# Performance work log

Measured on AMD Instinct MI355X. Metric: run time of the kernel, lower is better.

The kernel has to match this reference:

```python
import jax, jax.numpy as jnp
import numpy as np

ALPHA = 0.1  # config['alpha']


def setup_inputs() -> dict:
    key = jax.random.key(0)
    k1, k2, k3, k4, k5 = jax.random.split(key, 5)
    n_bs, bit, n_cls, class_bit, n_train = 128, 48, 100, 16, 10000
    u = jax.random.normal(k1, (n_bs, bit), dtype=jnp.float32)
    # multi-hot labels (float, as in torch: y.float())
    y = jax.random.bernoulli(k2, 0.1, (n_bs, n_cls)).astype(jnp.float32)
    ind = jnp.arange(n_bs, dtype=jnp.int64)  # distinct in-range row indices
    # buffers mid-training: U holds previous class-wise codes, Y previous labels
    U = jax.random.normal(k3, (n_train, n_cls, class_bit), dtype=jnp.float32) * 0.1
    Y = jax.random.bernoulli(k4, 0.1, (n_train, n_cls)).astype(jnp.float32)
    # xavier_uniform-like init for w_D [n_class, bit, class_bit]
    limit = np.sqrt(6.0 / (bit + class_bit)).astype(np.float32)
    w_D = jax.random.uniform(k5, (n_cls, bit, class_bit), dtype=jnp.float32,
                             minval=-limit, maxval=limit)
    return {"u": u, "y": y, "ind": ind, "U": U, "Y": Y, "w_D": w_D}


def reference(u, y, ind, U, Y, w_D):
    # update label buffer: self.Y[ind, :] = y
    Y = Y.at[ind].set(y)
    # u_ = matmul(u, w_D).permute(1,0,2): [n_bs, n_cls, class_bit]
    u_ = jnp.einsum('bk,ckd->bcd', u, w_D)
    # update code buffer with detached u_ (torch: self.U[ind] = u_.data)
    U = U.at[ind].set(jax.lax.stop_gradient(u_))
    # pairwise similarity s: [n_bs, n_train, n_cls]
    s = y[:, None, :] * Y[None, :, :]
    # inner_product: sum over class_bit -> [n_bs, n_train, n_cls]
    ip = jnp.einsum('tcd,bcd->btc', U, u_)
    # stable log(1 + exp(ip)) - s*ip, exactly as the torch expression
    likelihood = (jnp.log1p(jnp.exp(-jnp.abs(ip))) + jnp.maximum(ip, 0.0)
                  - s * ip).mean()
    quantization = ALPHA * jnp.mean((u_ - jnp.sign(u_)) ** 2)
    return likelihood + quantization
```

## Files before the change

kernel.cpp:

```cpp
#include <hip/hip_runtime.h>
#include <math.h>

#define CB 16
#define ALPHA 0.1f
#define LOG2E 1.4426950408889634f
#define LN2F  0.6931471805599453f

typedef __bf16 bf16x8 __attribute__((ext_vector_type(8)));
typedef float  f32x16 __attribute__((ext_vector_type(16)));

__device__ inline float block_reduce_256(float v, float* red) {
    #pragma unroll
    for (int off = 32; off > 0; off >>= 1) v += __shfl_down(v, off, 64);
    int lane = threadIdx.x & 63;
    int wid  = threadIdx.x >> 6;
    if (lane == 0) red[wid] = v;
    __syncthreads();
    float s = 0.f;
    if (threadIdx.x == 0) {
        int nw = blockDim.x >> 6;
        for (int w = 0; w < nw; ++w) s += red[w];
    }
    return s;
}

__global__ __launch_bounds__(256) void prep_kernel(
        const float* __restrict__ u, const float* __restrict__ y,
        const float* __restrict__ w_D,
        float* __restrict__ u_f32, __bf16* __restrict__ u_bf,
        float* __restrict__ quant_partials,
        float* __restrict__ vvec, float* __restrict__ wvec,
        int n_bs, int bit, int n_cls, int nub) {
    __shared__ float red[4];
    __shared__ float yus[4][64];
    __shared__ float sus[4][64];
    if ((int)blockIdx.x < nub) {
        int idx = blockIdx.x * 256 + threadIdx.x;
        int total = n_bs * n_cls * CB;
        float q = 0.f;
        if (idx < total) {
            int d = idx & (CB - 1);
            int c = (idx / CB) % n_cls;
            int b = idx / (CB * n_cls);
            const float* __restrict__ ur = u + (size_t)b * bit;
            const float* __restrict__ w  = w_D + (size_t)c * bit * CB + d;
            float s = 0.f;
            for (int k = 0; k < bit; ++k) s = fmaf(ur[k], w[k * CB], s);
            u_f32[idx] = s;
            u_bf[((size_t)c * n_bs + b) * CB + d] = (__bf16)(s * LOG2E);
            float sgn = (s > 0.f) ? 1.f : ((s < 0.f) ? -1.f : 0.f);
            float dd = s - sgn;
            q = dd * dd;
        }
        float bs = block_reduce_256(q, red);
        if (threadIdx.x == 0) quant_partials[blockIdx.x] = bs;
    } else {
        const int c  = blockIdx.x - nub;
        const int kk = threadIdx.x & 63;
        const int sl = threadIdx.x >> 6;
        float yv = 0.f, sv = 0.f;
        if (kk < bit) {
            const int bpp = n_bs >> 2;
            for (int b = sl * bpp; b < (sl + 1) * bpp; ++b) {
                float uv = u[(size_t)b * bit + kk];
                sv += uv;
                yv = fmaf(y[(size_t)b * n_cls + c], uv, yv);
            }
        }
        yus[sl][kk] = yv; sus[sl][kk] = sv;
        __syncthreads();
        if (sl == 0 && kk < bit) {
            yus[0][kk] = yus[0][kk] + yus[1][kk] + yus[2][kk] + yus[3][kk];
            sus[0][kk] = sus[0][kk] + sus[1][kk] + sus[2][kk] + sus[3][kk];
        }
        __syncthreads();
        if (threadIdx.x < CB) {
            const int d = threadIdx.x;
            const float* __restrict__ wdc = w_D + (size_t)c * bit * CB + d;
            float v = 0.f, w = 0.f;
            for (int k = 0; k < bit; ++k) {
                float wv = wdc[k * CB];
                v = fmaf(yus[0][k], wv, v);
                w = fmaf(sus[0][k], wv, w);
            }
            vvec[(size_t)c * CB + d] = v;
            wvec[(size_t)c * CB + d] = w;
        }
    }
}

__global__ __launch_bounds__(256, 4) void loss_main_mfma(
        const float* __restrict__ y, const float* __restrict__ U,
        const float* __restrict__ Yb, const float* __restrict__ u_f32,
        const __bf16* __restrict__ u_bf,
        const float* __restrict__ vvec, const float* __restrict__ wvec,
        const int* __restrict__ ind, float* __restrict__ partials,
        int n_bs, int n_cls, int n_train) {
    __shared__ float red[4];
    __shared__ int pflag[32];
    const int tid  = threadIdx.x;
    const int lane = tid & 63;
    const int wid  = tid >> 6;
    const int c    = blockIdx.x * 4 + wid;
    const int t0   = blockIdx.y * 32;
    const int r    = lane & 31;
    const int h    = lane >> 5;
    const int row  = t0 + r;

    if (tid < 32) pflag[tid] = -1;

    const int rc = (row < n_train) ? row : (n_train - 1);
    const float* __restrict__ ar = U + ((size_t)rc * n_cls + c) * CB + h * 8;
    float4 a0 = *(const float4*)(ar);
    float4 a1 = *(const float4*)(ar + 4);
    float Yv = Yb[(size_t)rc * n_cls + c];

    __syncthreads();
    if (tid < n_bs) {
        unsigned rl = (unsigned)(ind[tid] - t0);
        if (rl < 32u) pflag[rl] = tid;
    }
    __syncthreads();

    const int pf = pflag[r];
    if (pf >= 0) {
        const float* __restrict__ src =
            u_f32 + ((size_t)pf * n_cls + c) * CB + h * 8;
        a0 = *(const float4*)(src);
        a1 = *(const float4*)(src + 4);
        Yv = y[(size_t)pf * n_cls + c];
    }
    if (row >= n_train) {
        a0 = make_float4(0.f, 0.f, 0.f, 0.f); a1 = a0; Yv = 0.f;
    }

    const float* __restrict__ vp = vvec + (size_t)c * CB + h * 8;
    const float* __restrict__ wp = wvec + (size_t)c * CB + h * 8;
    float sv = a0.x*vp[0] + a0.y*vp[1] + a0.z*vp[2] + a0.w*vp[3]
             + a1.x*vp[4] + a1.y*vp[5] + a1.z*vp[6] + a1.w*vp[7];
    float sw = a0.x*wp[0] + a0.y*wp[1] + a0.z*wp[2] + a0.w*wp[3]
             + a1.x*wp[4] + a1.y*wp[5] + a1.z*wp[6] + a1.w*wp[7];
    const float sideS = Yv * sv;
    const float sideW = sw;

    bf16x8 A;
    A[0] = (__bf16)a0.x; A[1] = (__bf16)a0.y;
    A[2] = (__bf16)a0.z; A[3] = (__bf16)a0.w;
    A[4] = (__bf16)a1.x; A[5] = (__bf16)a1.y;
    A[6] = (__bf16)a1.z; A[7] = (__bf16)a1.w;

    const __bf16* __restrict__ ub = u_bf + (size_t)c * n_bs * CB;
    bf16x8 B[4];
    #pragma unroll
    for (int bt = 0; bt < 4; ++bt)
        B[bt] = *(const bf16x8*)(ub + (size_t)(bt * 32 + r) * CB + h * 8);

    float accA = 0.f;
    float pp   = 1.f;
    f32x16 zc = {};
    #pragma unroll
    for (int bt = 0; bt < 4; ++bt) {
        f32x16 D = __builtin_amdgcn_mfma_f32_32x32x16_bf16(A, B[bt], zc, 0, 0, 0);
        float a[16];
        #pragma unroll
        for (int j = 0; j < 16; ++j) {
            float ipa = fabsf(D[j]);
            a[j] = 1.0f + __builtin_amdgcn_exp2f(-ipa);
            accA += ipa;
        }
        #pragma unroll
        for (int s = 1; s < 16; s <<= 1)
            #pragma unroll
            for (int j = 0; j < 16; j += 2 * s) a[j] *= a[j + s];
        pp *= a[0];
    }
    float accL = __builtin_amdgcn_logf(pp);

    float contrib = LN2F * accL + (0.5f * LN2F) * accA + 0.5f * sideW - sideS;

    #pragma unroll
    for (int off = 32; off > 0; off >>= 1)
        contrib += __shfl_down(contrib, off, 64);
    if (lane == 0) red[wid] = contrib;
    __syncthreads();
    if (tid == 0) {
        int bid = blockIdx.y * gridDim.x + blockIdx.x;
        partials[bid] = red[0] + red[1] + red[2] + red[3];
    }
}

__global__ __launch_bounds__(256) void finalize_kernel(
        const float* __restrict__ partials, int nblk,
        const float* __restrict__ quant_partials, int n_quant,
        float* __restrict__ out, double pad_corr,
        double like_scale, double quant_scale) {
    double s = 0.0, q = 0.0;
    for (int i = threadIdx.x; i < nblk; i += 256) s += (double)partials[i];
    for (int i = threadIdx.x; i < n_quant; i += 256) q += (double)quant_partials[i];
    #pragma unroll
    for (int off = 32; off > 0; off >>= 1) {
        s += __shfl_down(s, off, 64);
        q += __shfl_down(q, off, 64);
    }
    __shared__ double dred[4][2];
    int lane = threadIdx.x & 63, wid = threadIdx.x >> 6;
    if (lane == 0) { dred[wid][0] = s; dred[wid][1] = q; }
    __syncthreads();
    if (threadIdx.x == 0) {
        double S = dred[0][0] + dred[1][0] + dred[2][0] + dred[3][0];
        double Q = dred[0][1] + dred[1][1] + dred[2][1] + dred[3][1];
        out[0] = (float)((S - pad_corr) * like_scale + Q * quant_scale);
    }
}

extern "C" void kernel_launch(void* const* d_in, const int* in_sizes, int n_in,
                              void* d_out, int out_size, void* d_ws, size_t ws_size,
                              hipStream_t stream) {
    const float* u   = (const float*)d_in[0];
    const float* y   = (const float*)d_in[1];
    const int*   ind = (const int*)d_in[2];
    const float* U   = (const float*)d_in[3];
    const float* Yb  = (const float*)d_in[4];
    const float* w_D = (const float*)d_in[5];

    const int n_bs    = in_sizes[2];
    const int bit     = in_sizes[0] / n_bs;
    const int n_cls   = in_sizes[1] / n_bs;
    const int n_train = in_sizes[4] / n_cls;

    const int totalU = n_bs * n_cls * CB;
    const int nub    = (totalU + 255) / 256;
    const int ntile  = (n_train + 31) / 32;
    const int gx     = (n_cls + 3) / 4;
    const int nblk   = ntile * gx;

    char* ws = (char*)d_ws;
    size_t off = 0;
    float* u_f32 = (float*)(ws + off);          off += (size_t)totalU * 4;
    __bf16* u_bf = (__bf16*)(ws + off);         off += (size_t)totalU * 2;
    off = (off + 15) & ~(size_t)15;
    float* vvec = (float*)(ws + off);           off += (size_t)n_cls * CB * 4;
    float* wvec = (float*)(ws + off);           off += (size_t)n_cls * CB * 4;
    float* quant_partials = (float*)(ws + off); off += (size_t)nub * 4;
    off = (off + 15) & ~(size_t)15;
    float* partials = (float*)(ws + off);       off += (size_t)nblk * 4;

    prep_kernel<<<nub + n_cls, 256, 0, stream>>>(
        u, y, w_D, u_f32, u_bf, quant_partials, vvec, wvec,
        n_bs, bit, n_cls, nub);

    loss_main_mfma<<<dim3(gx, ntile), 256, 0, stream>>>(
        y, U, Yb, u_f32, u_bf, vvec, wvec, ind, partials,
        n_bs, n_cls, n_train);

    const double ln2 = 0.6931471805599453;
    const double n_pad = (double)((long long)(ntile * 32 - n_train) *
                                  (long long)n_bs * (long long)n_cls);
    const double pad_corr    = ln2 * n_pad;
    const double like_scale  = 1.0 / ((double)n_bs * n_train * n_cls);
    const double quant_scale = (double)ALPHA / (double)totalU;

    finalize_kernel<<<1, 256, 0, stream>>>(partials, nblk, quant_partials, nub,
                                           (float*)d_out, pad_corr,
                                           like_scale, quant_scale);
}
```

Measured before the change: 51.21 us.

## Process four train tiles per block with register prefetch of next tile

Each block now loops over four 32-row train tiles instead of one. It loads the B fragments and the v/w vectors once per block and prefetches the next tile's U rows and labels into registers while the current tile runs its MFMAs and transcendentals. This amortizes per-block setup (index scan, B loads, syncs) and overlaps global loads with compute. The cost is four times fewer blocks (around 2500 instead of about 7800), which may reduce latency hiding from occupancy, and extra register pressure.

```diff
diff --git a/kernel.cpp b/kernel.cpp
--- a/kernel.cpp
+++ b/kernel.cpp
@@ -5,6 +5,7 @@
 #define ALPHA 0.1f
 #define LOG2E 1.4426950408889634f
 #define LN2F  0.6931471805599453f
+#define NT 4
 
 typedef __bf16 bf16x8 __attribute__((ext_vector_type(8)));
 typedef float  f32x16 __attribute__((ext_vector_type(16)));
@@ -97,86 +98,111 @@
         const int* __restrict__ ind, float* __restrict__ partials,
         int n_bs, int n_cls, int n_train) {
     __shared__ float red[4];
-    __shared__ int pflag[32];
+    __shared__ int pflag[NT * 32];
     const int tid  = threadIdx.x;
     const int lane = tid & 63;
     const int wid  = tid >> 6;
     const int c    = blockIdx.x * 4 + wid;
-    const int t0   = blockIdx.y * 32;
+    const int bt0  = blockIdx.y * (NT * 32);
     const int r    = lane & 31;
     const int h    = lane >> 5;
-    const int row  = t0 + r;
-
-    if (tid < 32) pflag[tid] = -1;
-
-    const int rc = (row < n_train) ? row : (n_train - 1);
-    const float* __restrict__ ar = U + ((size_t)rc * n_cls + c) * CB + h * 8;
-    float4 a0 = *(const float4*)(ar);
-    float4 a1 = *(const float4*)(ar + 4);
-    float Yv = Yb[(size_t)rc * n_cls + c];
-
+
+    for (int i = tid; i < NT * 32; i += 256) pflag[i] = -1;
     __syncthreads();
     if (tid < n_bs) {
-        unsigned rl = (unsigned)(ind[tid] - t0);
-        if (rl < 32u) pflag[rl] = tid;
-    }
-    __syncthreads();
-
-    const int pf = pflag[r];
-    if (pf >= 0) {
-        const float* __restrict__ src =
-            u_f32 + ((size_t)pf * n_cls + c) * CB + h * 8;
-        a0 = *(const float4*)(src);
-        a1 = *(const float4*)(src + 4);
-        Yv = y[(size_t)pf * n_cls + c];
-    }
-    if (row >= n_train) {
-        a0 = make_float4(0.f, 0.f, 0.f, 0.f); a1 = a0; Yv = 0.f;
-    }
+        unsigned rl = (unsigned)(ind[tid] - bt0);
+        if (rl < (unsigned)(NT * 32)) pflag[rl] = tid;
+    }
+
+    const __bf16* __restrict__ ub = u_bf + (size_t)c * n_bs * CB;
+    bf16x8 B[4];
+    #pragma unroll
+    for (int bt = 0; bt < 4; ++bt)
+        B[bt] = *(const bf16x8*)(ub + (size_t)(bt * 32 + r) * CB + h * 8);
 
     const float* __restrict__ vp = vvec + (size_t)c * CB + h * 8;
     const float* __restrict__ wp = wvec + (size_t)c * CB + h * 8;
-    float sv = a0.x*vp[0] + a0.y*vp[1] + a0.z*vp[2] + a0.w*vp[3]
-             + a1.x*vp[4] + a1.y*vp[5] + a1.z*vp[6] + a1.w*vp[7];
-    float sw = a0.x*wp[0] + a0.y*wp[1] + a0.z*wp[2] + a0.w*wp[3]
-             + a1.x*wp[4] + a1.y*wp[5] + a1.z*wp[6] + a1.w*wp[7];
-    const float sideS = Yv * sv;
-    const float sideW = sw;
-
-    bf16x8 A;
-    A[0] = (__bf16)a0.x; A[1] = (__bf16)a0.y;
-    A[2] = (__bf16)a0.z; A[3] = (__bf16)a0.w;
-    A[4] = (__bf16)a1.x; A[5] = (__bf16)a1.y;
-    A[6] = (__bf16)a1.z; A[7] = (__bf16)a1.w;
-
-    const __bf16* __restrict__ ub = u_bf + (size_t)c * n_bs * CB;
-    bf16x8 B[4];
-    #pragma unroll
-    for (int bt = 0; bt < 4; ++bt)
-        B[bt] = *(const bf16x8*)(ub + (size_t)(bt * 32 + r) * CB + h * 8);
+    float4 vp0 = *(const float4*)(vp);
+    float4 vp1 = *(const float4*)(vp + 4);
+    float4 wp0 = *(const float4*)(wp);
+    float4 wp1 = *(const float4*)(wp + 4);
+
+    __syncthreads();
+
+    int rowp = bt0 + r;
+    int rcp  = (rowp < n_train) ? rowp : (n_train - 1);
+    const float* __restrict__ arp = U + ((size_t)rcp * n_cls + c) * CB + h * 8;
+    float4 a0c = *(const float4*)(arp);
+    float4 a1c = *(const float4*)(arp + 4);
+    float  Yvc = Yb[(size_t)rcp * n_cls + c];
 
     float accA = 0.f;
-    float pp   = 1.f;
+    float accL = 0.f;
+    float linC = 0.f;
     f32x16 zc = {};
-    #pragma unroll
-    for (int bt = 0; bt < 4; ++bt) {
-        f32x16 D = __builtin_amdgcn_mfma_f32_32x32x16_bf16(A, B[bt], zc, 0, 0, 0);
-        float a[16];
+
+    #pragma unroll
+    for (int it = 0; it < NT; ++it) {
+        float4 a0n, a1n; float Yvn = 0.f;
+        if (it + 1 < NT) {
+            int rown = bt0 + (it + 1) * 32 + r;
+            int rcn  = (rown < n_train) ? rown : (n_train - 1);
+            const float* __restrict__ arn =
+                U + ((size_t)rcn * n_cls + c) * CB + h * 8;
+            a0n = *(const float4*)(arn);
+            a1n = *(const float4*)(arn + 4);
+            Yvn = Yb[(size_t)rcn * n_cls + c];
+        }
+
+        const int pf = pflag[it * 32 + r];
+        if (pf >= 0) {
+            const float* __restrict__ src =
+                u_f32 + ((size_t)pf * n_cls + c) * CB + h * 8;
+            a0c = *(const float4*)(src);
+            a1c = *(const float4*)(src + 4);
+            Yvc = y[(size_t)pf * n_cls + c];
+        }
+        const int rowc = bt0 + it * 32 + r;
+        if (rowc >= n_train) {
+            a0c = make_float4(0.f, 0.f, 0.f, 0.f); a1c = a0c; Yvc = 0.f;
+        }
+
+        float sv = a0c.x*vp0.x + a0c.y*vp0.y + a0c.z*vp0.z + a0c.w*vp0.w
+                 + a1c.x*vp1.x + a1c.y*vp1.y + a1c.z*vp1.z + a1c.w*vp1.w;
+        float sw = a0c.x*wp0.x + a0c.y*wp0.y + a0c.z*wp0.z + a0c.w*wp0.w
+                 + a1c.x*wp1.x + a1c.y*wp1.y + a1c.z*wp1.z + a1c.w*wp1.w;
+        linC += 0.5f * sw - Yvc * sv;
+
+        bf16x8 A;
+        A[0] = (__bf16)a0c.x; A[1] = (__bf16)a0c.y;
+        A[2] = (__bf16)a0c.z; A[3] = (__bf16)a0c.w;
+        A[4] = (__bf16)a1c.x; A[5] = (__bf16)a1c.y;
+        A[6] = (__bf16)a1c.z; A[7] = (__bf16)a1c.w;
+
+        float pp = 1.f;
         #pragma unroll
-        for (int j = 0; j < 16; ++j) {
-            float ipa = fabsf(D[j]);
-            a[j] = 1.0f + __builtin_amdgcn_exp2f(-ipa);
-            accA += ipa;
-        }
-        #pragma unroll
-        for (int s = 1; s < 16; s <<= 1)
+        for (int bt = 0; bt < 4; ++bt) {
+            f32x16 D = __builtin_amdgcn_mfma_f32_32x32x16_bf16(A, B[bt], zc,
+                                                               0, 0, 0);
+            float a[16];
             #pragma unroll
-            for (int j = 0; j < 16; j += 2 * s) a[j] *= a[j + s];
-        pp *= a[0];
-    }
-    float accL = __builtin_amdgcn_logf(pp);
-
-    float contrib = LN2F * accL + (0.5f * LN2F) * accA + 0.5f * sideW - sideS;
+            for (int j = 0; j < 16; ++j) {
+                float ipa = fabsf(D[j]);
+                a[j] = 1.0f + __builtin_amdgcn_exp2f(-ipa);
+                accA += ipa;
+            }
+            #pragma unroll
+            for (int s = 1; s < 16; s <<= 1)
+                #pragma unroll
+                for (int j = 0; j < 16; j += 2 * s) a[j] *= a[j + s];
+            pp *= a[0];
+        }
+        accL += __builtin_amdgcn_logf(pp);
+
+        a0c = a0n; a1c = a1n; Yvc = Yvn;
+    }
+
+    float contrib = LN2F * accL + (0.5f * LN2F) * accA + linC;
 
     #pragma unroll
     for (int off = 32; off > 0; off >>= 1)
@@ -231,8 +257,9 @@
     const int totalU = n_bs * n_cls * CB;
     const int nub    = (totalU + 255) / 256;
     const int ntile  = (n_train + 31) / 32;
+    const int gy     = (ntile + NT - 1) / NT;
     const int gx     = (n_cls + 3) / 4;
-    const int nblk   = ntile * gx;
+    const int nblk   = gy * gx;
 
     char* ws = (char*)d_ws;
     size_t off = 0;
@@ -249,12 +276,12 @@
         u, y, w_D, u_f32, u_bf, quant_partials, vvec, wvec,
         n_bs, bit, n_cls, nub);
 
-    loss_main_mfma<<<dim3(gx, ntile), 256, 0, stream>>>(
+    loss_main_mfma<<<dim3(gx, gy), 256, 0, stream>>>(
         y, U, Yb, u_f32, u_bf, vvec, wvec, ind, partials,
         n_bs, n_cls, n_train);
 
     const double ln2 = 0.6931471805599453;
-    const double n_pad = (double)((long long)(ntile * 32 - n_train) *
+    const double n_pad = (double)((long long)(gy * NT * 32 - n_train) *
                                   (long long)n_bs * (long long)n_cls);
     const double pad_corr    = ln2 * n_pad;
     const double like_scale  = 1.0 / ((double)n_bs * n_train * n_cls);
```

New measurement: 201.3 us. +293.0%, slower.

## Make loss blocks persistent over multiple train tiles with per-wave partials

Applied to the files above, without the earlier changes.

Each block now loops over up to eight strided 32-row train tiles instead of handling one tile, so the grid shrinks from 313 to 40 rows of blocks. The B operand, the v/w vectors and the ind-to-row flag table are loaded once per block and reused across tiles. The final cross-wave LDS reduction and barrier are removed; each wave writes its own partial and the finalize kernel sums four times as many entries. Fewer blocks (25x40 = 1000) means less launch and setup overhead. The cost is less parallelism and a serial dependency chain per block, with no unrolling of the tile loop.

```diff
diff --git a/kernel.cpp b/kernel.cpp
--- a/kernel.cpp
+++ b/kernel.cpp
@@ -5,6 +5,7 @@
 #define ALPHA 0.1f
 #define LOG2E 1.4426950408889634f
 #define LN2F  0.6931471805599453f
+#define MAXW 8
 
 typedef __bf16 bf16x8 __attribute__((ext_vector_type(8)));
 typedef float  f32x16 __attribute__((ext_vector_type(16)));
@@ -95,97 +96,104 @@
         const __bf16* __restrict__ u_bf,
         const float* __restrict__ vvec, const float* __restrict__ wvec,
         const int* __restrict__ ind, float* __restrict__ partials,
-        int n_bs, int n_cls, int n_train) {
-    __shared__ float red[4];
-    __shared__ int pflag[32];
+        int n_bs, int n_cls, int n_train, int ntile, int GY) {
+    __shared__ int pflag[MAXW * 32];
     const int tid  = threadIdx.x;
     const int lane = tid & 63;
     const int wid  = tid >> 6;
     const int c    = blockIdx.x * 4 + wid;
-    const int t0   = blockIdx.y * 32;
+    const int by   = blockIdx.y;
     const int r    = lane & 31;
     const int h    = lane >> 5;
-    const int row  = t0 + r;
-
-    if (tid < 32) pflag[tid] = -1;
-
-    const int rc = (row < n_train) ? row : (n_train - 1);
-    const float* __restrict__ ar = U + ((size_t)rc * n_cls + c) * CB + h * 8;
-    float4 a0 = *(const float4*)(ar);
-    float4 a1 = *(const float4*)(ar + 4);
-    float Yv = Yb[(size_t)rc * n_cls + c];
-
+    const int nw   = (ntile - by + GY - 1) / GY;
+
+    for (int i = tid; i < MAXW * 32; i += 256) pflag[i] = -1;
     __syncthreads();
     if (tid < n_bs) {
-        unsigned rl = (unsigned)(ind[tid] - t0);
-        if (rl < 32u) pflag[rl] = tid;
-    }
-    __syncthreads();
-
-    const int pf = pflag[r];
-    if (pf >= 0) {
-        const float* __restrict__ src =
-            u_f32 + ((size_t)pf * n_cls + c) * CB + h * 8;
-        a0 = *(const float4*)(src);
-        a1 = *(const float4*)(src + 4);
-        Yv = y[(size_t)pf * n_cls + c];
-    }
-    if (row >= n_train) {
-        a0 = make_float4(0.f, 0.f, 0.f, 0.f); a1 = a0; Yv = 0.f;
-    }
-
+        int t = ind[tid];
+        for (int w = 0; w < nw; ++w) {
+            unsigned rl = (unsigned)(t - (by + w * GY) * 32);
+            if (rl < 32u) pflag[w * 32 + rl] = tid;
+        }
+    }
+    __syncthreads();
+
+    const __bf16* __restrict__ ub = u_bf + (size_t)c * n_bs * CB;
+    bf16x8 B[4];
+    #pragma unroll
+    for (int bt = 0; bt < 4; ++bt)
+        B[bt] = *(const bf16x8*)(ub + (size_t)(bt * 32 + r) * CB + h * 8);
     const float* __restrict__ vp = vvec + (size_t)c * CB + h * 8;
     const float* __restrict__ wp = wvec + (size_t)c * CB + h * 8;
-    float sv = a0.x*vp[0] + a0.y*vp[1] + a0.z*vp[2] + a0.w*vp[3]
-             + a1.x*vp[4] + a1.y*vp[5] + a1.z*vp[6] + a1.w*vp[7];
-    float sw = a0.x*wp[0] + a0.y*wp[1] + a0.z*wp[2] + a0.w*wp[3]
-             + a1.x*wp[4] + a1.y*wp[5] + a1.z*wp[6] + a1.w*wp[7];
-    const float sideS = Yv * sv;
-    const float sideW = sw;
-
-    bf16x8 A;
-    A[0] = (__bf16)a0.x; A[1] = (__bf16)a0.y;
-    A[2] = (__bf16)a0.z; A[3] = (__bf16)a0.w;
-    A[4] = (__bf16)a1.x; A[5] = (__bf16)a1.y;
-    A[6] = (__bf16)a1.z; A[7] = (__bf16)a1.w;
-
-    const __bf16* __restrict__ ub = u_bf + (size_t)c * n_bs * CB;
-    bf16x8 B[4];
-    #pragma unroll
-    for (int bt = 0; bt < 4; ++bt)
-        B[bt] = *(const bf16x8*)(ub + (size_t)(bt * 32 + r) * CB + h * 8);
-
-    float accA = 0.f;
-    float pp   = 1.f;
+    float4 vp0 = *(const float4*)(vp);
+    float4 vp1 = *(const float4*)(vp + 4);
+    float4 wp0 = *(const float4*)(wp);
+    float4 wp1 = *(const float4*)(wp + 4);
+
+    float acc = 0.f;
     f32x16 zc = {};
-    #pragma unroll
-    for (int bt = 0; bt < 4; ++bt) {
-        f32x16 D = __builtin_amdgcn_mfma_f32_32x32x16_bf16(A, B[bt], zc, 0, 0, 0);
-        float a[16];
+    #pragma unroll 1
+    for (int w = 0; w < nw; ++w) {
+        const int t0  = (by + w * GY) * 32;
+        const int row = t0 + r;
+        const int rc  = (row < n_train) ? row : (n_train - 1);
+        const float* __restrict__ ar = U + ((size_t)rc * n_cls + c) * CB + h * 8;
+        float4 a0 = *(const float4*)(ar);
+        float4 a1 = *(const float4*)(ar + 4);
+        float Yv = Yb[(size_t)rc * n_cls + c];
+
+        const int pf = pflag[w * 32 + r];
+        if (pf >= 0) {
+            const float* __restrict__ src =
+                u_f32 + ((size_t)pf * n_cls + c) * CB + h * 8;
+            a0 = *(const float4*)(src);
+            a1 = *(const float4*)(src + 4);
+            Yv = y[(size_t)pf * n_cls + c];
+        }
+        if (row >= n_train) {
+            a0 = make_float4(0.f, 0.f, 0.f, 0.f); a1 = a0; Yv = 0.f;
+        }
+
+        float sv = a0.x*vp0.x + a0.y*vp0.y + a0.z*vp0.z + a0.w*vp0.w
+                 + a1.x*vp1.x + a1.y*vp1.y + a1.z*vp1.z + a1.w*vp1.w;
+        float sw = a0.x*wp0.x + a0.y*wp0.y + a0.z*wp0.z + a0.w*wp0.w
+                 + a1.x*wp1.x + a1.y*wp1.y + a1.z*wp1.z + a1.w*wp1.w;
+
+        bf16x8 A;
+        A[0] = (__bf16)a0.x; A[1] = (__bf16)a0.y;
+        A[2] = (__bf16)a0.z; A[3] = (__bf16)a0.w;
+        A[4] = (__bf16)a1.x; A[5] = (__bf16)a1.y;
+        A[6] = (__bf16)a1.z; A[7] = (__bf16)a1.w;
+
+        float accA = 0.f;
+        float pp   = 1.f;
         #pragma unroll
-        for (int j = 0; j < 16; ++j) {
-            float ipa = fabsf(D[j]);
-            a[j] = 1.0f + __builtin_amdgcn_exp2f(-ipa);
-            accA += ipa;
-        }
-        #pragma unroll
-        for (int s = 1; s < 16; s <<= 1)
+        for (int bt = 0; bt < 4; ++bt) {
+            f32x16 D = __builtin_amdgcn_mfma_f32_32x32x16_bf16(A, B[bt], zc,
+                                                               0, 0, 0);
+            float a[16];
             #pragma unroll
-            for (int j = 0; j < 16; j += 2 * s) a[j] *= a[j + s];
-        pp *= a[0];
-    }
-    float accL = __builtin_amdgcn_logf(pp);
-
-    float contrib = LN2F * accL + (0.5f * LN2F) * accA + 0.5f * sideW - sideS;
+            for (int j = 0; j < 16; ++j) {
+                float ipa = fabsf(D[j]);
+                a[j] = 1.0f + __builtin_amdgcn_exp2f(-ipa);
+                accA += ipa;
+            }
+            #pragma unroll
+            for (int s = 1; s < 16; s <<= 1)
+                #pragma unroll
+                for (int j = 0; j < 16; j += 2 * s) a[j] *= a[j + s];
+            pp *= a[0];
+        }
+        float accL = __builtin_amdgcn_logf(pp);
+        acc += LN2F * accL + (0.5f * LN2F) * accA + 0.5f * sw - Yv * sv;
+    }
 
     #pragma unroll
     for (int off = 32; off > 0; off >>= 1)
-        contrib += __shfl_down(contrib, off, 64);
-    if (lane == 0) red[wid] = contrib;
-    __syncthreads();
-    if (tid == 0) {
-        int bid = blockIdx.y * gridDim.x + blockIdx.x;
-        partials[bid] = red[0] + red[1] + red[2] + red[3];
+        acc += __shfl_down(acc, off, 64);
+    if (lane == 0) {
+        int bid = by * gridDim.x + blockIdx.x;
+        partials[bid * 4 + wid] = acc;
     }
 }
 
@@ -231,8 +239,10 @@
     const int totalU = n_bs * n_cls * CB;
     const int nub    = (totalU + 255) / 256;
     const int ntile  = (n_train + 31) / 32;
+    const int GY     = (ntile + MAXW - 1) / MAXW;
     const int gx     = (n_cls + 3) / 4;
-    const int nblk   = ntile * gx;
+    const int nblk   = GY * gx;
+    const int npart  = nblk * 4;
 
     char* ws = (char*)d_ws;
     size_t off = 0;
@@ -243,15 +253,15 @@
     float* wvec = (float*)(ws + off);           off += (size_t)n_cls * CB * 4;
     float* quant_partials = (float*)(ws + off); off += (size_t)nub * 4;
     off = (off + 15) & ~(size_t)15;
-    float* partials = (float*)(ws + off);       off += (size_t)nblk * 4;
+    float* partials = (float*)(ws + off);       off += (size_t)npart * 4;
 
     prep_kernel<<<nub + n_cls, 256, 0, stream>>>(
         u, y, w_D, u_f32, u_bf, quant_partials, vvec, wvec,
         n_bs, bit, n_cls, nub);
 
-    loss_main_mfma<<<dim3(gx, ntile), 256, 0, stream>>>(
+    loss_main_mfma<<<dim3(gx, GY), 256, 0, stream>>>(
         y, U, Yb, u_f32, u_bf, vvec, wvec, ind, partials,
-        n_bs, n_cls, n_train);
+        n_bs, n_cls, n_train, ntile, GY);
 
     const double ln2 = 0.6931471805599453;
     const double n_pad = (double)((long long)(ntile * 32 - n_train) *
@@ -260,7 +270,7 @@
     const double like_scale  = 1.0 / ((double)n_bs * n_train * n_cls);
     const double quant_scale = (double)ALPHA / (double)totalU;
 
-    finalize_kernel<<<1, 256, 0, stream>>>(partials, nblk, quant_partials, nub,
+    finalize_kernel<<<1, 256, 0, stream>>>(partials, npart, quant_partials, nub,
                                            (float*)d_out, pad_corr,
                                            like_scale, quant_scale);
 }
```

After: 51.67 us. About the same (+0.9%).
